# Optimization experiments

Hardware: AMD Instinct MI355X
Metric: run time of the kernel (lower is better)

## Reference

```python
import jax, jax.numpy as jnp
import numpy as np

BETA = 3.0

def setup_inputs() -> dict:
    key = jax.random.key(0)
    k1, k2 = jax.random.split(key)
    B, C = 65536, 1000
    outputs = jax.random.normal(k1, (B, C), dtype=jnp.float32)
    targets = jax.random.randint(k2, (B,), 0, C, dtype=jnp.int64)
    cost_matrix = jnp.zeros((C, C), dtype=jnp.float32)
    return {"outputs": outputs, "targets": targets, "cost_matrix": cost_matrix}

def reference(outputs, targets, cost_matrix):
    # [B, C] log-probs, single stable pass
    log_probs = jax.nn.log_softmax(outputs, axis=1)
    predicted = jnp.argmax(log_probs, axis=1)  # [B]

    # Fused scatter-add replacing the per-sample Python loop:
    # cost_matrix[t, p] += 1 for each (t, p) pair (duplicates accumulate).
    cm = cost_matrix.at[targets, predicted].add(1.0)

    # Row-normalize: cm[i] * beta / max(1, sum(cm[i]))
    row_sum = jnp.sum(cm, axis=1, keepdims=True)  # [C, 1]
    cm_norm = cm * (BETA / jnp.maximum(1.0, row_sum))

    # gather log_probs[b, targets[b]] and cm_norm[targets[b], predicted[b]]
    gather_log_probs = jnp.take_along_axis(log_probs, targets[:, None], axis=1)[:, 0]  # [B]
    gather_costs = cm_norm[targets, predicted]  # [B]

    return -jnp.mean(gather_log_probs * gather_costs)
```

## Files before the change

### kernel.cpp

```cpp
#include <hip/hip_runtime.h>
#include <math.h>

#define CLS 1000
#define VEC_PER_ROW 250
#define BETA 3.0f
#define NPART 256

__global__ __launch_bounds__(256) void softmax_pass(
    const float* __restrict__ outputs,
    const int* __restrict__ targets,
    float* __restrict__ cm,
    float* __restrict__ logp,
    int* __restrict__ pred,
    int B)
{
    const int wave = threadIdx.x >> 6;
    const int lane = threadIdx.x & 63;
    const int row  = blockIdx.x * 4 + wave;
    if (row >= B) return;

    const float4* rp = (const float4*)(outputs + (size_t)row * CLS);

    float4 r[4];
#pragma unroll
    for (int k = 0; k < 4; ++k) {
        const int j = lane + 64 * k;
        if (j < VEC_PER_ROW) {
            r[k] = rp[j];
        } else {
            r[k] = make_float4(-INFINITY, -INFINITY, -INFINITY, -INFINITY);
        }
    }

    float m = -INFINITY;
#pragma unroll
    for (int k = 0; k < 4; ++k)
        m = fmaxf(m, fmaxf(fmaxf(r[k].x, r[k].y), fmaxf(r[k].z, r[k].w)));
#pragma unroll
    for (int off = 32; off; off >>= 1)
        m = fmaxf(m, __shfl_xor(m, off));

    float S  = 0.0f;
    int  idx = 0x7fffffff;
#pragma unroll
    for (int k = 0; k < 4; ++k) {
        const int base = (lane + 64 * k) * 4;
        const float* f = (const float*)&r[k];
#pragma unroll
        for (int c = 0; c < 4; ++c) {
            const float x = f[c];
            S += __expf(x - m);
            if (x == m) idx = min(idx, base + c);
        }
    }
#pragma unroll
    for (int off = 32; off; off >>= 1) {
        S   += __shfl_xor(S, off);
        idx  = min(idx, __shfl_xor(idx, off));
    }

    if (lane == 0) {
        const int t   = targets[row];
        const float xt = outputs[(size_t)row * CLS + t];
        logp[row] = xt - m - __logf(S);
        pred[row] = idx;
        atomicAdd(&cm[(size_t)t * CLS + idx], 1.0f);
    }
}

__global__ __launch_bounds__(256) void row_scale(
    const float* __restrict__ cm,
    float* __restrict__ scale)
{
    const int wave = threadIdx.x >> 6;
    const int lane = threadIdx.x & 63;
    const int row  = blockIdx.x * 4 + wave;
    if (row >= CLS) return;

    const float4* rp = (const float4*)(cm + (size_t)row * CLS);
    float s = 0.0f;
    for (int j = lane; j < VEC_PER_ROW; j += 64) {
        const float4 v = rp[j];
        s += v.x + v.y + v.z + v.w;
    }
#pragma unroll
    for (int off = 32; off; off >>= 1) s += __shfl_xor(s, off);
    if (lane == 0) scale[row] = BETA / fmaxf(1.0f, s);
}

__global__ __launch_bounds__(256) void finalize_partial(
    const float* __restrict__ cm,
    const float* __restrict__ scale,
    const float* __restrict__ logp,
    const int* __restrict__ pred,
    const int* __restrict__ targets,
    float* __restrict__ partial,
    int B)
{
    float v = 0.0f;
    for (int i = blockIdx.x * 256 + threadIdx.x; i < B; i += NPART * 256) {
        const int t = targets[i];
        const int p = pred[i];
        v += logp[i] * cm[(size_t)t * CLS + p] * scale[t];
    }
    const int lane = threadIdx.x & 63;
    const int wave = threadIdx.x >> 6;
#pragma unroll
    for (int off = 32; off; off >>= 1) v += __shfl_xor(v, off);

    __shared__ float ssum[4];
    if (lane == 0) ssum[wave] = v;
    __syncthreads();
    if (threadIdx.x == 0)
        partial[blockIdx.x] = ssum[0] + ssum[1] + ssum[2] + ssum[3];
}

__global__ __launch_bounds__(256) void finalize_reduce(
    const float* __restrict__ partial,
    float* __restrict__ out,
    int B)
{
    float v = (threadIdx.x < NPART) ? partial[threadIdx.x] : 0.0f;
    const int lane = threadIdx.x & 63;
    const int wave = threadIdx.x >> 6;
#pragma unroll
    for (int off = 32; off; off >>= 1) v += __shfl_xor(v, off);

    __shared__ float ssum[4];
    if (lane == 0) ssum[wave] = v;
    __syncthreads();
    if (threadIdx.x == 0)
        out[0] = -(ssum[0] + ssum[1] + ssum[2] + ssum[3]) / (float)B;
}

extern "C" void kernel_launch(void* const* d_in, const int* in_sizes, int n_in,
                              void* d_out, int out_size, void* d_ws, size_t ws_size,
                              hipStream_t stream)
{
    const float* outputs     = (const float*)d_in[0];
    const int*   targets     = (const int*)d_in[1];
    const float* cost_matrix = (const float*)d_in[2];
    const int B = in_sizes[1];

    char* ws = (char*)d_ws;
    float* cm      = (float*)(ws);
    float* logp    = (float*)(ws + 4000000);
    int*   pred    = (int*)  (ws + 4000000 + (size_t)B * 4);
    float* scale   = (float*)(ws + 4000000 + (size_t)B * 8);
    float* partial = (float*)(ws + 4000000 + (size_t)B * 8 + 4096);

    hipMemcpyAsync(cm, cost_matrix, (size_t)CLS * CLS * sizeof(float),
                   hipMemcpyDeviceToDevice, stream);

    softmax_pass<<<(B + 3) / 4, 256, 0, stream>>>(outputs, targets, cm, logp, pred, B);
    row_scale<<<(CLS + 3) / 4, 256, 0, stream>>>(cm, scale);
    finalize_partial<<<NPART, 256, 0, stream>>>(cm, scale, logp, pred, targets,
                                                partial, B);
    finalize_reduce<<<1, 256, 0, stream>>>(partial, (float*)d_out, B);
}
```

Baseline: 361.3 us.

## Split cost matrix into base plus counts and track row histograms

Instead of copying the cost matrix into the workspace and atomically incrementing it, the softmax pass now accumulates counts into a zeroed buffer and also counts per-target rows. The base matrix's row sums are computed once before the main pass, so the row_scale pass over the updated matrix is no longer needed. The finalize step recombines base plus counts. The softmax also switches to exp2/log2 with four split accumulators. The cost is an extra atomic per row and a few more gathers in finalize.

```diff
diff --git a/kernel.cpp b/kernel.cpp
--- a/kernel.cpp
+++ b/kernel.cpp
@@ -5,11 +5,13 @@
 #define VEC_PER_ROW 250
 #define BETA 3.0f
 #define NPART 256
+#define LOG2E 1.44269504088896f
 
 __global__ __launch_bounds__(256) void softmax_pass(
     const float* __restrict__ outputs,
     const int* __restrict__ targets,
-    float* __restrict__ cm,
+    float* __restrict__ count,
+    float* __restrict__ h,
     float* __restrict__ logp,
     int* __restrict__ pred,
     int B)
@@ -40,19 +42,22 @@
     for (int off = 32; off; off >>= 1)
         m = fmaxf(m, __shfl_xor(m, off));
 
-    float S  = 0.0f;
-    int  idx = 0x7fffffff;
+    const float nmk = -m * LOG2E;
+    float s0 = 0.f, s1 = 0.f, s2 = 0.f, s3 = 0.f;
+    int idx = 0x7fffffff;
 #pragma unroll
     for (int k = 0; k < 4; ++k) {
         const int base = (lane + 64 * k) * 4;
-        const float* f = (const float*)&r[k];
-#pragma unroll
-        for (int c = 0; c < 4; ++c) {
-            const float x = f[c];
-            S += __expf(x - m);
-            if (x == m) idx = min(idx, base + c);
-        }
+        s0 += exp2f(fmaf(r[k].x, LOG2E, nmk));
+        s1 += exp2f(fmaf(r[k].y, LOG2E, nmk));
+        s2 += exp2f(fmaf(r[k].z, LOG2E, nmk));
+        s3 += exp2f(fmaf(r[k].w, LOG2E, nmk));
+        if (r[k].x == m) idx = min(idx, base);
+        if (r[k].y == m) idx = min(idx, base + 1);
+        if (r[k].z == m) idx = min(idx, base + 2);
+        if (r[k].w == m) idx = min(idx, base + 3);
     }
+    float S = (s0 + s1) + (s2 + s3);
 #pragma unroll
     for (int off = 32; off; off >>= 1) {
         S   += __shfl_xor(S, off);
@@ -60,24 +65,25 @@
     }
 
     if (lane == 0) {
-        const int t   = targets[row];
+        const int t    = targets[row];
         const float xt = outputs[(size_t)row * CLS + t];
-        logp[row] = xt - m - __logf(S);
+        logp[row] = xt - m - __log2f(S) * (1.0f / LOG2E);
         pred[row] = idx;
-        atomicAdd(&cm[(size_t)t * CLS + idx], 1.0f);
+        atomicAdd(&count[(size_t)t * CLS + idx], 1.0f);
+        atomicAdd(&h[t], 1.0f);
     }
 }
 
-__global__ __launch_bounds__(256) void row_scale(
-    const float* __restrict__ cm,
-    float* __restrict__ scale)
+__global__ __launch_bounds__(256) void rowsum0_kernel(
+    const float* __restrict__ cost0,
+    float* __restrict__ rowsum0)
 {
     const int wave = threadIdx.x >> 6;
     const int lane = threadIdx.x & 63;
     const int row  = blockIdx.x * 4 + wave;
     if (row >= CLS) return;
 
-    const float4* rp = (const float4*)(cm + (size_t)row * CLS);
+    const float4* rp = (const float4*)(cost0 + (size_t)row * CLS);
     float s = 0.0f;
     for (int j = lane; j < VEC_PER_ROW; j += 64) {
         const float4 v = rp[j];
@@ -85,12 +91,14 @@
     }
 #pragma unroll
     for (int off = 32; off; off >>= 1) s += __shfl_xor(s, off);
-    if (lane == 0) scale[row] = BETA / fmaxf(1.0f, s);
+    if (lane == 0) rowsum0[row] = s;
 }
 
 __global__ __launch_bounds__(256) void finalize_partial(
-    const float* __restrict__ cm,
-    const float* __restrict__ scale,
+    const float* __restrict__ count,
+    const float* __restrict__ cost0,
+    const float* __restrict__ h,
+    const float* __restrict__ rowsum0,
     const float* __restrict__ logp,
     const int* __restrict__ pred,
     const int* __restrict__ targets,
@@ -101,7 +109,10 @@
     for (int i = blockIdx.x * 256 + threadIdx.x; i < B; i += NPART * 256) {
         const int t = targets[i];
         const int p = pred[i];
-        v += logp[i] * cm[(size_t)t * CLS + p] * scale[t];
+        const size_t cell = (size_t)t * CLS + p;
+        const float cm  = count[cell] + cost0[cell];
+        const float rs  = rowsum0[t] + h[t];
+        v += logp[i] * cm * (BETA / fmaxf(1.0f, rs));
     }
     const int lane = threadIdx.x & 63;
     const int wave = threadIdx.x >> 6;
@@ -137,24 +148,25 @@
                               void* d_out, int out_size, void* d_ws, size_t ws_size,
                               hipStream_t stream)
 {
-    const float* outputs     = (const float*)d_in[0];
-    const int*   targets     = (const int*)d_in[1];
-    const float* cost_matrix = (const float*)d_in[2];
+    const float* outputs = (const float*)d_in[0];
+    const int*   targets = (const int*)d_in[1];
+    const float* cost0   = (const float*)d_in[2];
     const int B = in_sizes[1];
 
     char* ws = (char*)d_ws;
-    float* cm      = (float*)(ws);
-    float* logp    = (float*)(ws + 4000000);
-    int*   pred    = (int*)  (ws + 4000000 + (size_t)B * 4);
-    float* scale   = (float*)(ws + 4000000 + (size_t)B * 8);
-    float* partial = (float*)(ws + 4000000 + (size_t)B * 8 + 4096);
+    float* count   = (float*)(ws);
+    float* h       = (float*)(ws + 4000000);
+    float* logp    = (float*)(ws + 4004096);
+    int*   pred    = (int*)  (ws + 4004096 + (size_t)B * 4);
+    float* rowsum0 = (float*)(ws + 4004096 + (size_t)B * 8);
+    float* partial = (float*)(ws + 4004096 + (size_t)B * 8 + 4096);
 
-    hipMemcpyAsync(cm, cost_matrix, (size_t)CLS * CLS * sizeof(float),
-                   hipMemcpyDeviceToDevice, stream);
+    hipMemsetAsync(count, 0, 4004096, stream);
 
-    softmax_pass<<<(B + 3) / 4, 256, 0, stream>>>(outputs, targets, cm, logp, pred, B);
-    row_scale<<<(CLS + 3) / 4, 256, 0, stream>>>(cm, scale);
-    finalize_partial<<<NPART, 256, 0, stream>>>(cm, scale, logp, pred, targets,
-                                                partial, B);
+    rowsum0_kernel<<<(CLS + 3) / 4, 256, 0, stream>>>(cost0, rowsum0);
+    softmax_pass<<<(B + 3) / 4, 256, 0, stream>>>(outputs, targets, count, h,
+                                                  logp, pred, B);
+    finalize_partial<<<NPART, 256, 0, stream>>>(count, cost0, h, rowsum0,
+                                                logp, pred, targets, partial, B);
     finalize_reduce<<<1, 256, 0, stream>>>(partial, (float*)d_out, B);
 }
```

New measurement: 362.0 us. About the same (+0.2%).
